# Optimization experiments

Measured on AMD Instinct MI355X. Metric: run time of the kernel, lower is better.

## Reference

```python
import jax, jax.numpy as jnp
import numpy as np

LN_EPS = 1e-5


def layernorm(x, g, b):
    mu = jnp.mean(x, axis=-1, keepdims=True)
    var = jnp.mean((x - mu) ** 2, axis=-1, keepdims=True)
    return (x - mu) * jax.lax.rsqrt(var + LN_EPS) * g + b


def attention(x, qkv_w, proj_w, proj_b, num_heads):
    B, N, C = x.shape
    d = C // num_heads
    qkv = jnp.einsum('bnc,oc->bno', x, qkv_w)            # [B,N,3C], no bias (qkv_bias=False)
    qkv = qkv.reshape(B, N, num_heads, 3 * d).transpose(0, 2, 1, 3)  # [B,h,N,3d]
    q, k, v = qkv[..., :d], qkv[..., d:2 * d], qkv[..., 2 * d:]
    scores = jnp.einsum('bhnd,bhmd->bhnm', q, k) * (d ** -0.5)
    a = jax.nn.softmax(scores, axis=-1)
    o = jnp.einsum('bhnm,bhmd->bhnd', a, v).transpose(0, 2, 1, 3).reshape(B, N, C)
    return jnp.einsum('bnc,oc->bno', o, proj_w) + proj_b


def dwconv(x, w, b, H, W):
    # x: [B,N,C] -> NCHW depthwise 3x3 conv, stride 1, pad 1 -> [B,N,C]
    B, N, C = x.shape
    xi = x.transpose(0, 2, 1).reshape(B, C, H, W)
    y = jax.lax.conv_general_dilated(
        xi, w, window_strides=(1, 1), padding='SAME',
        dimension_numbers=('NCHW', 'OIHW', 'NCHW'), feature_group_count=C)
    y = y + b[None, :, None, None]
    return y.reshape(B, C, H * W).transpose(0, 2, 1)


def mlp(x, fc1_w, fc1_b, dw_w, dw_b, fc2_w, fc2_b, H, W):
    h = jnp.einsum('bnc,oc->bno', x, fc1_w) + fc1_b
    h = dwconv(h, dw_w, dw_b, H, W)
    h = jax.nn.gelu(h, approximate=False)  # torch nn.GELU default = exact erf
    return jnp.einsum('bnh,oh->bno', h, fc2_w) + fc2_b


def setup_inputs() -> dict:
    key = jax.random.key(0)
    ks = jax.random.split(key, 8)
    B, N, C, HID = 8, 1024, 512, 2048
    s = 0.02
    return {
        'x': jax.random.normal(ks[0], (B, N, C), jnp.float32),
        'ln1_g': jnp.ones((C,), jnp.float32),
        'ln1_b': jnp.zeros((C,), jnp.float32),
        'qkv_w': jax.random.normal(ks[1], (3 * C, C), jnp.float32) * s,
        'proj_w': jax.random.normal(ks[2], (C, C), jnp.float32) * s,
        'proj_b': jnp.zeros((C,), jnp.float32),
        'ln2_g': jnp.ones((C,), jnp.float32),
        'ln2_b': jnp.zeros((C,), jnp.float32),
        'fc1_w': jax.random.normal(ks[3], (HID, C), jnp.float32) * s,
        'fc1_b': jnp.zeros((HID,), jnp.float32),
        'dw_w': jax.random.normal(ks[4], (HID, 1, 3, 3), jnp.float32) * s,
        'dw_b': jnp.zeros((HID,), jnp.float32),
        'fc2_w': jax.random.normal(ks[5], (C, HID), jnp.float32) * s,
        'fc2_b': jnp.zeros((C,), jnp.float32),
        'H': 32,
        'W': 32,
    }


def reference(x, ln1_g, ln1_b, qkv_w, proj_w, proj_b, ln2_g, ln2_b,
              fc1_w, fc1_b, dw_w, dw_b, fc2_w, fc2_b, H, W):
    NUM_HEADS = 8
    x = x + attention(layernorm(x, ln1_g, ln1_b), qkv_w, proj_w, proj_b, NUM_HEADS)
    x = x + mlp(layernorm(x, ln2_g, ln2_b), fc1_w, fc1_b, dw_w, dw_b, fc2_w, fc2_b, H, W)
    return x
```

## Files before the change

### kernel.cpp

```cpp
#include <hip/hip_runtime.h>
#include <hip/hip_bf16.h>


typedef __attribute__((ext_vector_type(8))) short short8;
typedef __attribute__((ext_vector_type(4))) short s16x4;
typedef __attribute__((ext_vector_type(4))) float f32x4;

__device__ __forceinline__ float b2f(short s) {
    union { float f; unsigned u; } z; z.u = ((unsigned)(unsigned short)s) << 16; return z.f;
}
__device__ __forceinline__ short f2b(float f) {
    union { float f; unsigned u; } z; z.f = f;
    unsigned r = (z.u + 0x7fffu + ((z.u >> 16) & 1u)) >> 16;
    return (short)r;
}

__device__ __forceinline__ void gload_lds16(const void* g, void* l) {
    __builtin_amdgcn_global_load_lds(
        (const __attribute__((address_space(1))) void*)g,
        (__attribute__((address_space(3))) void*)l, 16, 0, 0);
}

__global__ __launch_bounds__(256) void cvt_weights(
    const float* __restrict__ s0, const float* __restrict__ s1,
    const float* __restrict__ s2, const float* __restrict__ s3,
    short* __restrict__ d0, short* __restrict__ d1,
    short* __restrict__ d2, short* __restrict__ d3) {
    long i = (long)blockIdx.x * 256 + threadIdx.x;
    const float* s; short* d; long off;
    if (i < 196608)      { s = s0; d = d0; off = i; }
    else if (i < 262144) { s = s1; d = d1; off = i - 196608; }
    else if (i < 524288) { s = s2; d = d2; off = i - 262144; }
    else                 { s = s3; d = d3; off = i - 524288; }
    float4 v = ((const float4*)s)[off];
    ushort4 o;
    o.x = (unsigned short)f2b(v.x); o.y = (unsigned short)f2b(v.y);
    o.z = (unsigned short)f2b(v.z); o.w = (unsigned short)f2b(v.w);
    ((ushort4*)d)[off] = o;
}

__global__ __launch_bounds__(256) void cvt_dw(
    const float* __restrict__ src, float* __restrict__ dst) {
    int i = blockIdx.x * 256 + threadIdx.x;
    int t = i >> 11, c = i & 2047;
    dst[t * 2048 + c] = src[c * 9 + t];
}

__global__ __launch_bounds__(256) void ln_kernel(
    const float* __restrict__ x, const float* __restrict__ g,
    const float* __restrict__ b, short* __restrict__ y) {
    int row  = blockIdx.x * 4 + (threadIdx.x >> 6);
    int lane = threadIdx.x & 63;
    const float* xr = x + (long)row * 512 + lane * 8;
    float4 v0 = ((const float4*)xr)[0];
    float4 v1 = ((const float4*)xr)[1];
    float e0[8] = {v0.x, v0.y, v0.z, v0.w, v1.x, v1.y, v1.z, v1.w};
    float s = 0.f;
#pragma unroll
    for (int e = 0; e < 8; e++) s += e0[e];
#pragma unroll
    for (int d = 1; d < 64; d <<= 1) s += __shfl_xor(s, d);
    float mu = s * (1.0f / 512.0f);
    float q = 0.f;
#pragma unroll
    for (int e = 0; e < 8; e++) { float t = e0[e] - mu; q += t * t; }
#pragma unroll
    for (int d = 1; d < 64; d <<= 1) q += __shfl_xor(q, d);
    float rs = rsqrtf(q * (1.0f / 512.0f) + 1e-5f);
    const float* gp = g + lane * 8;
    const float* bp = b + lane * 8;
    short8 o;
#pragma unroll
    for (int e = 0; e < 8; e++) o[e] = f2b((e0[e] - mu) * rs * gp[e] + bp[e]);
    *(short8*)(y + (long)row * 512 + lane * 8) = o;
}

template <typename Epi>
__global__ __launch_bounds__(256, 2) void gemm_bt(
    const short* __restrict__ A, const short* __restrict__ B, int K, Epi epi) {
    __shared__ short As[128 * 32];
    __shared__ short Bs[128 * 32];
    int tid = threadIdx.x;
    int lane = tid & 63, w = tid >> 6;
    int lr = lane & 15, lq = lane >> 4;
    int wm = (w & 1) * 64, wn = (w >> 1) * 64;
    long r0 = (long)blockIdx.x * 128, o0 = (long)blockIdx.y * 128;
    f32x4 acc[4][4];
#pragma unroll
    for (int i = 0; i < 4; i++)
#pragma unroll
        for (int j = 0; j < 4; j++) acc[i][j] = (f32x4){0.f, 0.f, 0.f, 0.f};
    const short* Ab = A + r0 * K;
    const short* Bb = B + o0 * K;
    int row = tid >> 2;
    int col = (tid & 3) * 8;
    for (int k0 = 0; k0 < K; k0 += 32) {
        gload_lds16(Ab + (long)row * K + k0 + col,        As + w * 512);
        gload_lds16(Ab + (long)(row + 64) * K + k0 + col, As + (w + 4) * 512);
        gload_lds16(Bb + (long)row * K + k0 + col,        Bs + w * 512);
        gload_lds16(Bb + (long)(row + 64) * K + k0 + col, Bs + (w + 4) * 512);
        __syncthreads();
        short8 af[4], bfr[4];
#pragma unroll
        for (int i = 0; i < 4; i++)
            af[i] = *(const short8*)&As[(wm + i * 16 + lr) * 32 + lq * 8];
#pragma unroll
        for (int j = 0; j < 4; j++)
            bfr[j] = *(const short8*)&Bs[(wn + j * 16 + lr) * 32 + lq * 8];
#pragma unroll
        for (int i = 0; i < 4; i++)
#pragma unroll
            for (int j = 0; j < 4; j++)
                acc[i][j] = __builtin_amdgcn_mfma_f32_16x16x32_bf16(
                    af[i], bfr[j], acc[i][j], 0, 0, 0);
        __syncthreads();
    }
#pragma unroll
    for (int i = 0; i < 4; i++)
#pragma unroll
        for (int j = 0; j < 4; j++)
#pragma unroll
            for (int rg = 0; rg < 4; rg++)
                epi((int)(r0 + wm + i * 16 + lq * 4 + rg),
                    (int)(o0 + wn + j * 16 + lr), acc[i][j][rg]);
}

struct EpiQKV {
    short *q, *k, *vt;
    __device__ void operator()(int r, int o, float v) const {
        int b = r >> 10, n = r & 1023;
        int h = o / 192, j = o - h * 192;
        int bh = b * 8 + h;
        short bv = f2b(v);
        if (j < 64)        q[((long)bh * 1024 + n) * 64 + j] = bv;
        else if (j < 128)  k[((long)bh * 1024 + n) * 64 + (j - 64)] = bv;
        else               vt[((long)bh * 64 + (j - 128)) * 1024 + n] = bv;
    }
};
struct EpiProj {
    const float* pb; const float* x; float* x1;
    __device__ void operator()(int r, int o, float v) const {
        long idx = (long)r * 512 + o;
        x1[idx] = v + pb[o] + x[idx];
    }
};
struct EpiBias {
    const float* bias; short* out; int O;
    __device__ void operator()(int r, int o, float v) const {
        out[(long)r * O + o] = f2b(v + bias[o]);
    }
};
struct EpiFc2 {
    const float* bias; const float* x1; float* out;
    __device__ void operator()(int r, int o, float v) const {
        long idx = (long)r * 512 + o;
        out[idx] = v + bias[o] + x1[idx];
    }
};

__global__ __launch_bounds__(256, 2) void attn_kernel(
    const short* __restrict__ Q, const short* __restrict__ K,
    const short* __restrict__ Vt, short* __restrict__ out) {
    __shared__ __align__(16) char smem[53248];
    int bh = blockIdx.x, qb = blockIdx.y;
    int tid = threadIdx.x, w = tid >> 6, lane = tid & 63;
    int lr = lane & 15, lq = lane >> 4;
    short* Kt = (short*)(smem + w * 13312);
    short* Vl = (short*)(smem + w * 13312 + 4096);
    short* Pt = (short*)(smem + w * 13312 + 8192);
    short* Oshb = (short*)smem;
    float* Lsh  = (float*)(smem + 36864);

    const short* Qb = Q + ((long)bh * 1024 + qb * 64) * 64;
    const short* Kb = K + (long)bh * 1024 * 64;
    const short* Vb = Vt + (long)bh * 64 * 1024;

    short8 qf[4][2];
#pragma unroll
    for (int jt = 0; jt < 4; jt++)
#pragma unroll
        for (int ks = 0; ks < 2; ks++)
            qf[jt][ks] = *(const short8*)(Qb + (jt * 16 + lr) * 64 + ks * 32 + lq * 8);

    f32x4 oacc[4][4];
#pragma unroll
    for (int mt = 0; mt < 4; mt++)
#pragma unroll
        for (int dt = 0; dt < 4; dt++) oacc[mt][dt] = (f32x4){0.f, 0.f, 0.f, 0.f};
    float lsum[4] = {0.f, 0.f, 0.f, 0.f};

    for (int it = 0; it < 8; it++) {
        int n0 = w * 256 + it * 32;
#pragma unroll
        for (int i = 0; i < 4; i++) {
            int s = i * 64 + lane;
            int row = s >> 3, ch = (s & 7) ^ (row & 7);
            gload_lds16(Kb + (long)(n0 + row) * 64 + ch * 8, Kt + i * 512);
        }
#pragma unroll
        for (int i = 0; i < 4; i++) {
            int s = i * 64 + lane;
            int row = s >> 2, ch = s & 3;
            gload_lds16(Vb + (long)row * 1024 + n0 + ch * 8, Vl + i * 512);
        }
        asm volatile("s_waitcnt vmcnt(0)" ::: "memory");
        f32x4 sacc[2][4];
#pragma unroll
        for (int kt = 0; kt < 2; kt++)
#pragma unroll
            for (int jt = 0; jt < 4; jt++) sacc[kt][jt] = (f32x4){0.f, 0.f, 0.f, 0.f};
#pragma unroll
        for (int ks = 0; ks < 2; ks++)
#pragma unroll
            for (int kt = 0; kt < 2; kt++) {
                short8 ak = *(const short8*)&Kt[(kt * 16 + lr) * 64 +
                                                (((ks * 4 + lq) ^ (lr & 7)) * 8)];
#pragma unroll
                for (int jt = 0; jt < 4; jt++)
                    sacc[kt][jt] = __builtin_amdgcn_mfma_f32_16x16x32_bf16(
                        ak, qf[jt][ks], sacc[kt][jt], 0, 0, 0);
            }
#pragma unroll
        for (int kt = 0; kt < 2; kt++)
#pragma unroll
            for (int jt = 0; jt < 4; jt++) {
                s16x4 pv;
#pragma unroll
                for (int rg = 0; rg < 4; rg++) {
                    float e = __expf(sacc[kt][jt][rg] * 0.125f);
                    lsum[jt] += e;
                    pv[rg] = f2b(e);
                }
                *(s16x4*)&Pt[(jt * 16 + lr) * 40 + kt * 16 + lq * 4] = pv;
            }
        short8 bv[4];
#pragma unroll
        for (int dt = 0; dt < 4; dt++)
            bv[dt] = *(const short8*)&Vl[(dt * 16 + lr) * 32 + lq * 8];
#pragma unroll
        for (int mt = 0; mt < 4; mt++) {
            short8 ap = *(const short8*)&Pt[(mt * 16 + lr) * 40 + lq * 8];
#pragma unroll
            for (int dt = 0; dt < 4; dt++)
                oacc[mt][dt] = __builtin_amdgcn_mfma_f32_16x16x32_bf16(
                    ap, bv[dt], oacc[mt][dt], 0, 0, 0);
        }
    }
#pragma unroll
    for (int jt = 0; jt < 4; jt++) {
        lsum[jt] += __shfl_xor(lsum[jt], 16);
        lsum[jt] += __shfl_xor(lsum[jt], 32);
    }
    __syncthreads();
#pragma unroll
    for (int mt = 0; mt < 4; mt++)
#pragma unroll
        for (int dt = 0; dt < 4; dt++)
#pragma unroll
            for (int rg = 0; rg < 4; rg++)
                Oshb[w * 4608 + (mt * 16 + lq * 4 + rg) * 72 + dt * 16 + lr] =
                    f2b(oacc[mt][dt][rg]);
    if (lq == 0)
#pragma unroll
        for (int jt = 0; jt < 4; jt++) Lsh[w * 64 + jt * 16 + lr] = lsum[jt];
    __syncthreads();
    int m = tid >> 2, dg = (tid & 3) * 16;
    float l = Lsh[m] + Lsh[64 + m] + Lsh[128 + m] + Lsh[192 + m];
    float inv = 1.0f / l;
    float r[16];
#pragma unroll
    for (int i = 0; i < 16; i++) r[i] = 0.f;
#pragma unroll
    for (int ww = 0; ww < 4; ww++) {
        const short8* op = (const short8*)&Oshb[ww * 4608 + m * 72 + dg];
        short8 a = op[0], bq = op[1];
#pragma unroll
        for (int i = 0; i < 8; i++) { r[i] += b2f(a[i]); r[8 + i] += b2f(bq[i]); }
    }
    short8 o0, o1;
#pragma unroll
    for (int i = 0; i < 8; i++) { o0[i] = f2b(r[i] * inv); o1[i] = f2b(r[8 + i] * inv); }
    int b = bh >> 3, h = bh & 7;
    long base = ((long)(b * 1024 + qb * 64 + m)) * 512 + h * 64 + dg;
    *(short8*)(out + base) = o0;
    *(short8*)(out + base + 8) = o1;
}

__global__ __launch_bounds__(256) void dwconv_gelu(
    const short* __restrict__ h1, const float* __restrict__ wdT,
    const float* __restrict__ bias, short* __restrict__ h2) {
    int bn = blockIdx.x;
    int b = bn >> 10, n = bn & 1023;
    int yy = n >> 5, xx = n & 31;
    int c0 = threadIdx.x * 8;
    float4 bv0 = ((const float4*)&bias[c0])[0];
    float4 bv1 = ((const float4*)&bias[c0])[1];
    float acc[8] = {bv0.x, bv0.y, bv0.z, bv0.w, bv1.x, bv1.y, bv1.z, bv1.w};
    for (int ky = 0; ky < 3; ky++) {
        int ys = yy + ky - 1;
        if (ys < 0 || ys > 31) continue;
        for (int kx = 0; kx < 3; kx++) {
            int xs = xx + kx - 1;
            if (xs < 0 || xs > 31) continue;
            short8 hv = *(const short8*)&h1[((long)(b * 1024 + ys * 32 + xs)) * 2048 + c0];
            const float4* wp = (const float4*)&wdT[(ky * 3 + kx) * 2048 + c0];
            float4 wa = wp[0], wb = wp[1];
            float wv[8] = {wa.x, wa.y, wa.z, wa.w, wb.x, wb.y, wb.z, wb.w};
#pragma unroll
            for (int e = 0; e < 8; e++)
                acc[e] += b2f(hv[e]) * wv[e];
        }
    }
    short8 o;
#pragma unroll
    for (int e = 0; e < 8; e++) {
        float a = acc[e];
        o[e] = f2b(0.5f * a * (1.0f + erff(a * 0.70710678118f)));
    }
    *(short8*)&h2[((long)bn) * 2048 + c0] = o;
}

extern "C" void kernel_launch(void* const* d_in, const int* in_sizes, int n_in,
                              void* d_out, int out_size, void* d_ws, size_t ws_size,
                              hipStream_t stream) {
    const float* x      = (const float*)d_in[0];
    const float* ln1_g  = (const float*)d_in[1];
    const float* ln1_b  = (const float*)d_in[2];
    const float* qkv_w  = (const float*)d_in[3];
    const float* proj_w = (const float*)d_in[4];
    const float* proj_b = (const float*)d_in[5];
    const float* ln2_g  = (const float*)d_in[6];
    const float* ln2_b  = (const float*)d_in[7];
    const float* fc1_w  = (const float*)d_in[8];
    const float* fc1_b  = (const float*)d_in[9];
    const float* dw_w   = (const float*)d_in[10];
    const float* dw_b   = (const float*)d_in[11];
    const float* fc2_w  = (const float*)d_in[12];
    const float* fc2_b  = (const float*)d_in[13];
    float* out = (float*)d_out;

    char* p = (char*)d_ws;
    short* wq   = (short*)p; p += (long)1536 * 512 * 2;
    short* wp   = (short*)p; p += (long)512 * 512 * 2;
    short* w1   = (short*)p; p += (long)2048 * 512 * 2;
    short* w2   = (short*)p; p += (long)512 * 2048 * 2;
    float* wdT  = (float*)p; p += (long)9 * 2048 * 4;
    short* y1   = (short*)p; p += (long)8192 * 512 * 2;
    short* q    = (short*)p; p += (long)64 * 1024 * 64 * 2;
    short* k    = (short*)p; p += (long)64 * 1024 * 64 * 2;
    short* vt   = (short*)p; p += (long)64 * 64 * 1024 * 2;
    short* attn = (short*)p; p += (long)8192 * 512 * 2;
    float* x1   = (float*)p; p += (long)8192 * 512 * 4;
    short* y2   = (short*)p; p += (long)8192 * 512 * 2;
    short* h1   = (short*)p; p += (long)8192 * 2048 * 2;
    short* h2   = (short*)p; p += (long)8192 * 2048 * 2;
    if ((size_t)(p - (char*)d_ws) > ws_size) return;

    cvt_weights<<<3072, 256, 0, stream>>>(qkv_w, proj_w, fc1_w, fc2_w, wq, wp, w1, w2);
    cvt_dw<<<72, 256, 0, stream>>>(dw_w, wdT);
    ln_kernel<<<2048, 256, 0, stream>>>(x, ln1_g, ln1_b, y1);
    gemm_bt<EpiQKV><<<dim3(64, 12), 256, 0, stream>>>(y1, wq, 512, EpiQKV{q, k, vt});
    attn_kernel<<<dim3(64, 16), 256, 0, stream>>>(q, k, vt, attn);
    gemm_bt<EpiProj><<<dim3(64, 4), 256, 0, stream>>>(attn, wp, 512, EpiProj{proj_b, x, x1});
    ln_kernel<<<2048, 256, 0, stream>>>(x1, ln2_g, ln2_b, y2);
    gemm_bt<EpiBias><<<dim3(64, 16), 256, 0, stream>>>(y2, w1, 512, EpiBias{fc1_b, h1, 2048});
    dwconv_gelu<<<8192, 256, 0, stream>>>(h1, wdT, dw_b, h2);
    gemm_bt<EpiFc2><<<dim3(64, 4), 256, 0, stream>>>(h2, w2, 2048, EpiFc2{fc2_b, x1, out});
}
```

Baseline: 317.3 us.

## Triple-buffer A tile in swizzled LDS and stream B fragments from global

The GEMM main loop now keeps three LDS buffers for the A tile and prefetches the next K-slice while computing the current one. It synchronises with a single raw s_barrier and an explicit vmcnt wait, instead of two __syncthreads per step. A rows use an XOR swizzle to reduce LDS bank conflicts. B fragments skip LDS entirely and are loaded straight from global memory into registers one step ahead, which trades LDS traffic for duplicated, strided global loads across the waves that share a column block.

```diff
diff --git a/kernel.cpp b/kernel.cpp
--- a/kernel.cpp
+++ b/kernel.cpp
@@ -78,8 +78,7 @@
 template <typename Epi>
 __global__ __launch_bounds__(256, 2) void gemm_bt(
     const short* __restrict__ A, const short* __restrict__ B, int K, Epi epi) {
-    __shared__ short As[128 * 32];
-    __shared__ short Bs[128 * 32];
+    __shared__ short As[3][128 * 32];
     int tid = threadIdx.x;
     int lane = tid & 63, w = tid >> 6;
     int lr = lane & 15, lq = lane >> 4;
@@ -92,28 +91,50 @@
         for (int j = 0; j < 4; j++) acc[i][j] = (f32x4){0.f, 0.f, 0.f, 0.f};
     const short* Ab = A + r0 * K;
     const short* Bb = B + o0 * K;
-    int row = tid >> 2;
-    int col = (tid & 3) * 8;
-    for (int k0 = 0; k0 < K; k0 += 32) {
-        gload_lds16(Ab + (long)row * K + k0 + col,        As + w * 512);
-        gload_lds16(Ab + (long)(row + 64) * K + k0 + col, As + (w + 4) * 512);
-        gload_lds16(Bb + (long)row * K + k0 + col,        Bs + w * 512);
-        gload_lds16(Bb + (long)(row + 64) * K + k0 + col, Bs + (w + 4) * 512);
-        __syncthreads();
-        short8 af[4], bfr[4];
-#pragma unroll
-        for (int i = 0; i < 4; i++)
-            af[i] = *(const short8*)&As[(wm + i * 16 + lr) * 32 + lq * 8];
-#pragma unroll
-        for (int j = 0; j < 4; j++)
-            bfr[j] = *(const short8*)&Bs[(wn + j * 16 + lr) * 32 + lq * 8];
+    int sr0 = w * 16 + (lane >> 2);
+    int sr1 = sr0 + 64;
+    int sc0 = ((lane & 3) ^ ((sr0 >> 1) & 3)) * 8;
+    int sc1 = ((lane & 3) ^ ((sr1 >> 1) & 3)) * 8;
+    const short* Bl = Bb + (long)(wn + lr) * K + lq * 8;
+
+    gload_lds16(Ab + (long)sr0 * K + sc0, &As[0][w * 512]);
+    gload_lds16(Ab + (long)sr1 * K + sc1, &As[0][(w + 4) * 512]);
+    short8 bcur[4];
+#pragma unroll
+    for (int j = 0; j < 4; j++)
+        bcur[j] = *(const short8*)(Bl + (long)j * 16 * K);
+
+    int nsteps = K >> 5;
+    int cb = 0;
+    for (int s = 0; s < nsteps; s++) {
+        int k0 = s << 5;
+        int nb = cb + 1; if (nb == 3) nb = 0;
+        if (s + 1 < nsteps) {
+            gload_lds16(Ab + (long)sr0 * K + k0 + 32 + sc0, &As[nb][w * 512]);
+            gload_lds16(Ab + (long)sr1 * K + k0 + 32 + sc1, &As[nb][(w + 4) * 512]);
+            asm volatile("s_waitcnt vmcnt(6)" ::: "memory");
+        } else {
+            asm volatile("s_waitcnt vmcnt(0)" ::: "memory");
+        }
+        asm volatile("s_barrier" ::: "memory");
+        short8 af[4];
+#pragma unroll
+        for (int i = 0; i < 4; i++) {
+            int row = wm + i * 16 + lr;
+            af[i] = *(const short8*)&As[cb][row * 32 + ((lq ^ ((row >> 1) & 3)) * 8)];
+        }
 #pragma unroll
         for (int i = 0; i < 4; i++)
 #pragma unroll
             for (int j = 0; j < 4; j++)
                 acc[i][j] = __builtin_amdgcn_mfma_f32_16x16x32_bf16(
-                    af[i], bfr[j], acc[i][j], 0, 0, 0);
-        __syncthreads();
+                    af[i], bcur[j], acc[i][j], 0, 0, 0);
+        if (s + 1 < nsteps) {
+#pragma unroll
+            for (int j = 0; j < 4; j++)
+                bcur[j] = *(const short8*)(Bl + (long)j * 16 * K + k0 + 32);
+        }
+        cb = nb;
     }
 #pragma unroll
     for (int i = 0; i < 4; i++)
```

Result: slower. 356.4 us (+12.3%).

## Split-K proj/fc2 GEMMs with atomic accumulation and swizzle LDS tiles

Applied to the files above, without the earlier changes.

The proj and fc2 GEMMs, which launch only 256 blocks, are now split four ways along K via a z grid dimension. Partial results go into the output with atomicAdd, after a new prefill kernel writes bias plus residual into that output. The LDS tile layout also gets an XOR swizzle on the column chunk to cut bank conflicts, and launch bounds rise to 4 blocks per CU. In exchange there are extra prefill launches, atomic traffic, and summation order that is no longer deterministic.

```diff
diff --git a/kernel.cpp b/kernel.cpp
--- a/kernel.cpp
+++ b/kernel.cpp
@@ -46,6 +46,17 @@
     dst[t * 2048 + c] = src[c * 9 + t];
 }
 
+__global__ __launch_bounds__(256) void prefill_bias_res(
+    const float* __restrict__ src, const float* __restrict__ bias,
+    float* __restrict__ dst) {
+    long i = (long)blockIdx.x * 256 + threadIdx.x;
+    int o4 = (int)(i & 127);
+    float4 s = ((const float4*)src)[i];
+    float4 bv = ((const float4*)bias)[o4];
+    float4 d = {s.x + bv.x, s.y + bv.y, s.z + bv.z, s.w + bv.w};
+    ((float4*)dst)[i] = d;
+}
+
 __global__ __launch_bounds__(256) void ln_kernel(
     const float* __restrict__ x, const float* __restrict__ g,
     const float* __restrict__ b, short* __restrict__ y) {
@@ -76,8 +87,9 @@
 }
 
 template <typename Epi>
-__global__ __launch_bounds__(256, 2) void gemm_bt(
-    const short* __restrict__ A, const short* __restrict__ B, int K, Epi epi) {
+__global__ __launch_bounds__(256, 4) void gemm_bt(
+    const short* __restrict__ A, const short* __restrict__ B, int K, int kloc,
+    Epi epi) {
     __shared__ short As[128 * 32];
     __shared__ short Bs[128 * 32];
     int tid = threadIdx.x;
@@ -85,6 +97,7 @@
     int lr = lane & 15, lq = lane >> 4;
     int wm = (w & 1) * 64, wn = (w >> 1) * 64;
     long r0 = (long)blockIdx.x * 128, o0 = (long)blockIdx.y * 128;
+    int kbase = blockIdx.z * kloc;
     f32x4 acc[4][4];
 #pragma unroll
     for (int i = 0; i < 4; i++)
@@ -92,21 +105,25 @@
         for (int j = 0; j < 4; j++) acc[i][j] = (f32x4){0.f, 0.f, 0.f, 0.f};
     const short* Ab = A + r0 * K;
     const short* Bb = B + o0 * K;
-    int row = tid >> 2;
-    int col = (tid & 3) * 8;
-    for (int k0 = 0; k0 < K; k0 += 32) {
-        gload_lds16(Ab + (long)row * K + k0 + col,        As + w * 512);
-        gload_lds16(Ab + (long)(row + 64) * K + k0 + col, As + (w + 4) * 512);
-        gload_lds16(Bb + (long)row * K + k0 + col,        Bs + w * 512);
-        gload_lds16(Bb + (long)(row + 64) * K + k0 + col, Bs + (w + 4) * 512);
+    int srow = tid >> 2;
+    int sc = ((tid & 3) ^ ((srow >> 1) & 3)) * 8;
+    for (int k0 = kbase; k0 < kbase + kloc; k0 += 32) {
+        gload_lds16(Ab + (long)srow * K + k0 + sc,        As + w * 512);
+        gload_lds16(Ab + (long)(srow + 64) * K + k0 + sc, As + (w + 4) * 512);
+        gload_lds16(Bb + (long)srow * K + k0 + sc,        Bs + w * 512);
+        gload_lds16(Bb + (long)(srow + 64) * K + k0 + sc, Bs + (w + 4) * 512);
         __syncthreads();
         short8 af[4], bfr[4];
 #pragma unroll
-        for (int i = 0; i < 4; i++)
-            af[i] = *(const short8*)&As[(wm + i * 16 + lr) * 32 + lq * 8];
-#pragma unroll
-        for (int j = 0; j < 4; j++)
-            bfr[j] = *(const short8*)&Bs[(wn + j * 16 + lr) * 32 + lq * 8];
+        for (int i = 0; i < 4; i++) {
+            int row = wm + i * 16 + lr;
+            af[i] = *(const short8*)&As[row * 32 + ((lq ^ ((row >> 1) & 3)) * 8)];
+        }
+#pragma unroll
+        for (int j = 0; j < 4; j++) {
+            int row = wn + j * 16 + lr;
+            bfr[j] = *(const short8*)&Bs[row * 32 + ((lq ^ ((row >> 1) & 3)) * 8)];
+        }
 #pragma unroll
         for (int i = 0; i < 4; i++)
 #pragma unroll
@@ -137,24 +154,16 @@
         else               vt[((long)bh * 64 + (j - 128)) * 1024 + n] = bv;
     }
 };
-struct EpiProj {
-    const float* pb; const float* x; float* x1;
-    __device__ void operator()(int r, int o, float v) const {
-        long idx = (long)r * 512 + o;
-        x1[idx] = v + pb[o] + x[idx];
-    }
-};
 struct EpiBias {
     const float* bias; short* out; int O;
     __device__ void operator()(int r, int o, float v) const {
         out[(long)r * O + o] = f2b(v + bias[o]);
     }
 };
-struct EpiFc2 {
-    const float* bias; const float* x1; float* out;
+struct EpiAtomic {
+    float* dst;
     __device__ void operator()(int r, int o, float v) const {
-        long idx = (long)r * 512 + o;
-        out[idx] = v + bias[o] + x1[idx];
+        atomicAdd(dst + (long)r * 512 + o, v);
     }
 };
 
@@ -359,11 +368,17 @@
     cvt_weights<<<3072, 256, 0, stream>>>(qkv_w, proj_w, fc1_w, fc2_w, wq, wp, w1, w2);
     cvt_dw<<<72, 256, 0, stream>>>(dw_w, wdT);
     ln_kernel<<<2048, 256, 0, stream>>>(x, ln1_g, ln1_b, y1);
-    gemm_bt<EpiQKV><<<dim3(64, 12), 256, 0, stream>>>(y1, wq, 512, EpiQKV{q, k, vt});
+    gemm_bt<EpiQKV><<<dim3(64, 12, 1), 256, 0, stream>>>(y1, wq, 512, 512,
+                                                         EpiQKV{q, k, vt});
     attn_kernel<<<dim3(64, 16), 256, 0, stream>>>(q, k, vt, attn);
-    gemm_bt<EpiProj><<<dim3(64, 4), 256, 0, stream>>>(attn, wp, 512, EpiProj{proj_b, x, x1});
+    prefill_bias_res<<<4096, 256, 0, stream>>>(x, proj_b, x1);
+    gemm_bt<EpiAtomic><<<dim3(64, 4, 4), 256, 0, stream>>>(attn, wp, 512, 128,
+                                                           EpiAtomic{x1});
     ln_kernel<<<2048, 256, 0, stream>>>(x1, ln2_g, ln2_b, y2);
-    gemm_bt<EpiBias><<<dim3(64, 16), 256, 0, stream>>>(y2, w1, 512, EpiBias{fc1_b, h1, 2048});
+    gemm_bt<EpiBias><<<dim3(64, 16, 1), 256, 0, stream>>>(y2, w1, 512, 512,
+                                                          EpiBias{fc1_b, h1, 2048});
     dwconv_gelu<<<8192, 256, 0, stream>>>(h1, wdT, dw_b, h2);
-    gemm_bt<EpiFc2><<<dim3(64, 4), 256, 0, stream>>>(h2, w2, 2048, EpiFc2{fc2_b, x1, out});
-}
+    prefill_bias_res<<<4096, 256, 0, stream>>>(x1, fc2_b, out);
+    gemm_bt<EpiAtomic><<<dim3(64, 4, 4), 256, 0, stream>>>(h2, w2, 2048, 512,
+                                                           EpiAtomic{out});
+}
```

Result: slower. 371.7 us (+17.1%).

## Swizzle GEMM LDS layout and use 64-row tiles for narrow-output GEMMs

Applied to the files above, without the earlier changes.

Adds an XOR swizzle on the 16-byte chunk index for both the global-to-LDS stores and the fragment reads, to cut LDS bank conflicts. Templates the GEMM on the M tile size and switches the proj and fc2 GEMMs (512 outputs) to 64-row tiles. This doubles their grid from 256 to 512 blocks so more CUs get work. Launch bounds are raised to 4 blocks per SIMD, which caps registers per thread and trades data reuse per block for occupancy.

```diff
diff --git a/kernel.cpp b/kernel.cpp
--- a/kernel.cpp
+++ b/kernel.cpp
@@ -75,42 +75,49 @@
     *(short8*)(y + (long)row * 512 + lane * 8) = o;
 }
 
-template <typename Epi>
-__global__ __launch_bounds__(256, 2) void gemm_bt(
+template <int MT, typename Epi>
+__global__ __launch_bounds__(256, 4) void gemm_bt(
     const short* __restrict__ A, const short* __restrict__ B, int K, Epi epi) {
-    __shared__ short As[128 * 32];
+    constexpr int NJ = (MT == 128) ? 4 : 2;
+    __shared__ short As[MT * 32];
     __shared__ short Bs[128 * 32];
     int tid = threadIdx.x;
     int lane = tid & 63, w = tid >> 6;
     int lr = lane & 15, lq = lane >> 4;
-    int wm = (w & 1) * 64, wn = (w >> 1) * 64;
-    long r0 = (long)blockIdx.x * 128, o0 = (long)blockIdx.y * 128;
-    f32x4 acc[4][4];
+    int wm = (MT == 128) ? (w & 1) * 64 : 0;
+    int wn = (MT == 128) ? (w >> 1) * 64 : w * 32;
+    long r0 = (long)blockIdx.x * MT, o0 = (long)blockIdx.y * 128;
+    f32x4 acc[4][NJ];
 #pragma unroll
     for (int i = 0; i < 4; i++)
 #pragma unroll
-        for (int j = 0; j < 4; j++) acc[i][j] = (f32x4){0.f, 0.f, 0.f, 0.f};
+        for (int j = 0; j < NJ; j++) acc[i][j] = (f32x4){0.f, 0.f, 0.f, 0.f};
     const short* Ab = A + r0 * K;
     const short* Bb = B + o0 * K;
-    int row = tid >> 2;
-    int col = (tid & 3) * 8;
+    int srow = tid >> 2;
+    int sc = ((tid & 3) ^ ((srow >> 1) & 3)) * 8;
     for (int k0 = 0; k0 < K; k0 += 32) {
-        gload_lds16(Ab + (long)row * K + k0 + col,        As + w * 512);
-        gload_lds16(Ab + (long)(row + 64) * K + k0 + col, As + (w + 4) * 512);
-        gload_lds16(Bb + (long)row * K + k0 + col,        Bs + w * 512);
-        gload_lds16(Bb + (long)(row + 64) * K + k0 + col, Bs + (w + 4) * 512);
+        gload_lds16(Ab + (long)srow * K + k0 + sc, As + w * 512);
+        if (MT == 128)
+            gload_lds16(Ab + (long)(srow + 64) * K + k0 + sc, As + (w + 4) * 512);
+        gload_lds16(Bb + (long)srow * K + k0 + sc,        Bs + w * 512);
+        gload_lds16(Bb + (long)(srow + 64) * K + k0 + sc, Bs + (w + 4) * 512);
         __syncthreads();
-        short8 af[4], bfr[4];
+        short8 af[4], bfr[NJ];
+#pragma unroll
+        for (int i = 0; i < 4; i++) {
+            int row = wm + i * 16 + lr;
+            af[i] = *(const short8*)&As[row * 32 + ((lq ^ ((row >> 1) & 3)) * 8)];
+        }
+#pragma unroll
+        for (int j = 0; j < NJ; j++) {
+            int row = wn + j * 16 + lr;
+            bfr[j] = *(const short8*)&Bs[row * 32 + ((lq ^ ((row >> 1) & 3)) * 8)];
+        }
 #pragma unroll
         for (int i = 0; i < 4; i++)
-            af[i] = *(const short8*)&As[(wm + i * 16 + lr) * 32 + lq * 8];
-#pragma unroll
-        for (int j = 0; j < 4; j++)
-            bfr[j] = *(const short8*)&Bs[(wn + j * 16 + lr) * 32 + lq * 8];
-#pragma unroll
-        for (int i = 0; i < 4; i++)
-#pragma unroll
-            for (int j = 0; j < 4; j++)
+#pragma unroll
+            for (int j = 0; j < NJ; j++)
                 acc[i][j] = __builtin_amdgcn_mfma_f32_16x16x32_bf16(
                     af[i], bfr[j], acc[i][j], 0, 0, 0);
         __syncthreads();
@@ -118,7 +125,7 @@
 #pragma unroll
     for (int i = 0; i < 4; i++)
 #pragma unroll
-        for (int j = 0; j < 4; j++)
+        for (int j = 0; j < NJ; j++)
 #pragma unroll
             for (int rg = 0; rg < 4; rg++)
                 epi((int)(r0 + wm + i * 16 + lq * 4 + rg),
@@ -359,11 +366,14 @@
     cvt_weights<<<3072, 256, 0, stream>>>(qkv_w, proj_w, fc1_w, fc2_w, wq, wp, w1, w2);
     cvt_dw<<<72, 256, 0, stream>>>(dw_w, wdT);
     ln_kernel<<<2048, 256, 0, stream>>>(x, ln1_g, ln1_b, y1);
-    gemm_bt<EpiQKV><<<dim3(64, 12), 256, 0, stream>>>(y1, wq, 512, EpiQKV{q, k, vt});
+    gemm_bt<128><<<dim3(64, 12), 256, 0, stream>>>(y1, wq, 512, EpiQKV{q, k, vt});
     attn_kernel<<<dim3(64, 16), 256, 0, stream>>>(q, k, vt, attn);
-    gemm_bt<EpiProj><<<dim3(64, 4), 256, 0, stream>>>(attn, wp, 512, EpiProj{proj_b, x, x1});
+    gemm_bt<64><<<dim3(128, 4), 256, 0, stream>>>(attn, wp, 512,
+                                                  EpiProj{proj_b, x, x1});
     ln_kernel<<<2048, 256, 0, stream>>>(x1, ln2_g, ln2_b, y2);
-    gemm_bt<EpiBias><<<dim3(64, 16), 256, 0, stream>>>(y2, w1, 512, EpiBias{fc1_b, h1, 2048});
+    gemm_bt<128><<<dim3(64, 16), 256, 0, stream>>>(y2, w1, 512,
+                                                   EpiBias{fc1_b, h1, 2048});
     dwconv_gelu<<<8192, 256, 0, stream>>>(h1, wdT, dw_b, h2);
-    gemm_bt<EpiFc2><<<dim3(64, 4), 256, 0, stream>>>(h2, w2, 2048, EpiFc2{fc2_b, x1, out});
-}
+    gemm_bt<64><<<dim3(128, 4), 256, 0, stream>>>(h2, w2, 2048,
+                                                  EpiFc2{fc2_b, x1, out});
+}
```

After: 297.0 us. -6.4%, faster.
